# Kernel optimization log

Measured on AMD Instinct MI355X. Metric: run time of the kernel, lower is better.

The kernel has to match this reference:

```python
import jax, jax.numpy as jnp
import numpy as np

KERNEL_NUM = 21
SIGMA = 0.1
EXACT_SIGMA = 0.001

def _kernel_params():
    mus, sigmas = [], []
    for i in range(KERNEL_NUM):
        mu = 1.0 / (KERNEL_NUM - 1) + 2.0 * i / (KERNEL_NUM - 1) - 1.0
        sigma = SIGMA
        if mu > 1.0:
            sigma = EXACT_SIGMA
            mu = 1.0
        mus.append(mu)
        sigmas.append(sigma)
    return np.asarray(mus, np.float32), np.asarray(sigmas, np.float32)

MU, SIG = _kernel_params()  # [K], [K]

def setup_inputs() -> dict:
    key = jax.random.key(0)
    k = jax.random.split(key, 8)
    V, D, B, L, R = 50000, 128, 512, 30, 200
    emb = jax.random.normal(k[0], (V, D), dtype=jnp.float32)
    W = jax.random.normal(k[1], (1, KERNEL_NUM), dtype=jnp.float32) * 0.1
    b = jax.random.normal(k[2], (1,), dtype=jnp.float32) * 0.1
    query1 = jax.random.randint(k[3], (B, L), 0, V, dtype=jnp.int32)
    doc1 = jax.random.randint(k[4], (B, R), 0, V, dtype=jnp.int32)
    query2 = jax.random.randint(k[5], (B, L), 0, V, dtype=jnp.int32)
    doc2 = jax.random.randint(k[6], (B, R), 0, V, dtype=jnp.int32)
    return {"emb": emb, "W": W, "b": b, "query1": query1, "doc1": doc1,
            "query2": query2, "doc2": doc2}

def _l2norm(x):
    # F.normalize(p=2, dim=-1): x / max(||x||, eps)
    n = jnp.sqrt(jnp.sum(x * x, axis=-1, keepdims=True))
    return x / jnp.maximum(n, 1e-12)

def _predict(emb, W, b, q, d):
    eq = _l2norm(emb[q])              # [B,L,D]
    ed = _l2norm(emb[d])              # [B,R,D]
    M = jnp.einsum('bld,brd->blr', eq, ed)  # matching matrix [B,L,R]
    # multi-Gaussian kernel bank: [B,L,R,K]
    Kmat = jnp.exp(-0.5 * (M[..., None] - MU) ** 2 / (SIG ** 2))
    km = jnp.sum(jnp.log1p(jnp.sum(Kmat, axis=2)), axis=1)  # [B,K]
    return km @ W.T + b               # [B,1]

def reference(emb, W, b, query1, doc1, query2, doc2):
    logits1 = _predict(emb, W, b, query1, doc1)
    logits2 = _predict(emb, W, b, query2, doc2)
    return jax.nn.sigmoid(logits1 - logits2)
```

## Files before the change

kernel.cpp:

```cpp
#include <hip/hip_runtime.h>
#include <math.h>

#define V   50000
#define DIM 128
#define BB  512
#define LQ  30
#define RD  200
#define KN  21

typedef unsigned short ushort_t;
typedef __attribute__((ext_vector_type(8))) short bf16x8;
typedef __attribute__((ext_vector_type(4))) float f32x4;
typedef __attribute__((ext_vector_type(2))) float f32x2;

#if __has_builtin(__builtin_amdgcn_exp2f)
#define EXP2F(x) __builtin_amdgcn_exp2f(x)
#else
#define EXP2F(x) __expf((x) * 0.69314718f)
#endif

#define ALPHA 72.1347520f
#define E10   22026.4657948f

static __device__ __forceinline__ ushort_t f2bf(float x) {
    unsigned u = __builtin_bit_cast(unsigned, x);
    return (ushort_t)((u + 0x7FFFu + ((u >> 16) & 1u)) >> 16);
}
static __device__ __forceinline__ bf16x8 as_frag(int4 v) {
    return __builtin_bit_cast(bf16x8, v);
}

__global__ __launch_bounds__(256) void knrm_norm(const float* __restrict__ emb,
                                                 ushort_t* __restrict__ nh) {
    int row = blockIdx.x * 8 + (threadIdx.x >> 5);
    int c4  = (threadIdx.x & 31) * 4;
    const float4 v = *reinterpret_cast<const float4*>(emb + (size_t)row * DIM + c4);
    float ss = v.x * v.x + v.y * v.y + v.z * v.z + v.w * v.w;
#pragma unroll
    for (int off = 1; off < 32; off <<= 1) ss += __shfl_xor(ss, off);
    float inv = 1.0f / fmaxf(sqrtf(ss), 1e-12f);
    uint2 o;
    o.x = (unsigned)f2bf(v.x * inv) | ((unsigned)f2bf(v.y * inv) << 16);
    o.y = (unsigned)f2bf(v.z * inv) | ((unsigned)f2bf(v.w * inv) << 16);
    *reinterpret_cast<uint2*>(nh + (size_t)row * DIM + c4) = o;
}

static __device__ __forceinline__ void bank4_pk(f32x4 pv, int4 dt, int qt,
                                                f32x2* ks2, float& cnt) {
    const float mv[4] = {pv[0], pv[1], pv[2], pv[3]};
    const int   dv[4] = {dt.x, dt.y, dt.z, dt.w};
    f32x2 t[4], u[4];
#pragma unroll
    for (int i = 0; i < 4; ++i) {
        float m  = mv[i];
        float dA = m + 0.5f, dB = m - 0.5f;
        float tA = EXP2F(-ALPHA * dA * (dA + 0.9f));
        float tB = EXP2F(-ALPHA * dB * (dB + 0.9f));
        float uB = EXP2F(14.4269504f * dB);
        float uA = uB * E10;
        t[i] = f32x2{tA, tB};
        u[i] = f32x2{uA, uB};
        cnt += (dv[i] == qt) ? 1.0f : 0.0f;
    }
#pragma unroll
    for (int k = 0; k < 10; ++k) {
        ks2[k] += (t[0] + t[1]) + (t[2] + t[3]);
        t[0] *= u[0]; t[1] *= u[1]; t[2] *= u[2]; t[3] *= u[3];
    }
}

static __device__ __forceinline__ void load_frag4(const ushort_t* base, int4* f) {
    f[0] = *reinterpret_cast<const int4*>(base);
    f[1] = *reinterpret_cast<const int4*>(base + 32);
    f[2] = *reinterpret_cast<const int4*>(base + 64);
    f[3] = *reinterpret_cast<const int4*>(base + 96);
}

__global__ __launch_bounds__(256, 4) void knrm_main(
    const ushort_t* __restrict__ nh, const float* __restrict__ W,
    const int* __restrict__ q1, const int* __restrict__ d1,
    const int* __restrict__ q2, const int* __restrict__ d2,
    float* __restrict__ logits)
{
    __shared__ int sQtok[32];
    __shared__ __align__(16) int sDtok[256];
    __shared__ float kred[4][32][KN];

    const int pb = blockIdx.x;
    const int pair = pb >> 9, b = pb & 511;
    const int* qind = (pair ? q2 : q1) + b * LQ;
    const int* dind = (pair ? d2 : d1) + b * RD;

    const int tid = threadIdx.x;
    const int lane = tid & 63, w = tid >> 6;
    const int r = lane & 15, g = lane >> 4;

    if (tid < 32) sQtok[tid] = (tid < LQ) ? qind[tid] : -2;
    { int c = tid; sDtok[c] = (c < RD) ? dind[c] : -1; }

    const int qiA = qind[r];
    const int qiB = qind[(16 + r) < LQ ? (16 + r) : LQ - 1];
    int4 qa[4], qb[4];
    load_frag4(nh + (size_t)qiA * DIM + g * 8, qa);
    load_frag4(nh + (size_t)qiB * DIM + g * 8, qb);

    __syncthreads();

    const int qt0 = sQtok[r], qt1 = sQtok[16 + r];
    const int4* sDtok4 = (const int4*)sDtok;

    f32x2 ks0[10], ks1[10];
#pragma unroll
    for (int k = 0; k < 10; ++k) { ks0[k] = f32x2{0.f, 0.f}; ks1[k] = f32x2{0.f, 0.f}; }
    float cnt0 = 0.0f, cnt1 = 0.0f;

    const int ns = (w < 3) ? 4 : 1;
#pragma unroll 2
    for (int s = 0; s < ns; ++s) {
        const int sbase = w * 64 + s * 16;
        const int dcol = sbase + r;
        const int di = sDtok[dcol < RD ? dcol : RD - 1];

        int4 df[4];
        load_frag4(nh + (size_t)di * DIM + g * 8, df);

        f32x4 acc0 = {0.f, 0.f, 0.f, 0.f}, acc1 = {0.f, 0.f, 0.f, 0.f};
#pragma unroll
        for (int ks = 0; ks < 4; ++ks) {
            bf16x8 fd = as_frag(df[ks]);
            acc0 = __builtin_amdgcn_mfma_f32_16x16x32_bf16(fd, as_frag(qa[ks]), acc0, 0, 0, 0);
            acc1 = __builtin_amdgcn_mfma_f32_16x16x32_bf16(fd, as_frag(qb[ks]), acc1, 0, 0, 0);
        }

        if (sbase + g * 4 < RD) {
            const int4 dt = sDtok4[(sbase >> 2) + g];
            bank4_pk(acc0, dt, qt0, ks0, cnt0);
            bank4_pk(acc1, dt, qt1, ks1, cnt1);
        }
    }

#pragma unroll
    for (int k = 0; k < 10; ++k) {
        float a0 = ks0[k].x, b0 = ks0[k].y, a1 = ks1[k].x, b1 = ks1[k].y;
        a0 += __shfl_xor(a0, 16); a0 += __shfl_xor(a0, 32);
        b0 += __shfl_xor(b0, 16); b0 += __shfl_xor(b0, 32);
        a1 += __shfl_xor(a1, 16); a1 += __shfl_xor(a1, 32);
        b1 += __shfl_xor(b1, 16); b1 += __shfl_xor(b1, 32);
        ks0[k] = f32x2{a0, b0};
        ks1[k] = f32x2{a1, b1};
    }
    cnt0 += __shfl_xor(cnt0, 16); cnt0 += __shfl_xor(cnt0, 32);
    cnt1 += __shfl_xor(cnt1, 16); cnt1 += __shfl_xor(cnt1, 32);

    if (lane < 16) {
        float* k0 = &kred[w][r][0];
        float* k1 = &kred[w][16 + r][0];
#pragma unroll
        for (int k = 0; k < 10; ++k) {
            k0[k] = ks0[k].x;  k0[10 + k] = ks0[k].y;
            k1[k] = ks1[k].x;  k1[10 + k] = ks1[k].y;
        }
        k0[20] = cnt0;
        k1[20] = cnt1;
    }
    __syncthreads();

    if (lane < 32 && tid < 64) {  }
    if (tid < 64) {
        float part = 0.0f;
        if (tid < LQ) {
#pragma unroll
            for (int k = 0; k < KN; ++k) {
                float s = kred[0][tid][k] + kred[1][tid][k]
                        + kred[2][tid][k] + kred[3][tid][k];
                float sc = 1.0f;
                if (k < 20) {
                    float j = (float)((k < 10) ? k : k - 10) - 4.5f;
                    sc = EXP2F(-0.721347520f * j * j);
                }
                part += W[k] * log1pf(sc * s);
            }
        }
        part += __shfl_xor(part, 1);
        part += __shfl_xor(part, 2);
        part += __shfl_xor(part, 4);
        part += __shfl_xor(part, 8);
        part += __shfl_xor(part, 16);
        part += __shfl_xor(part, 32);
        if (tid == 0) logits[pair * BB + b] = part;
    }
}

__global__ void knrm_final(const float* __restrict__ logits, float* __restrict__ out) {
    int i = blockIdx.x * blockDim.x + threadIdx.x;
    if (i < BB) {
        float x = logits[i] - logits[BB + i];
        out[i] = 1.0f / (1.0f + expf(-x));
    }
}

extern "C" void kernel_launch(void* const* d_in, const int* in_sizes, int n_in,
                              void* d_out, int out_size, void* d_ws, size_t ws_size,
                              hipStream_t stream) {
    const float* emb = (const float*)d_in[0];
    const float* W   = (const float*)d_in[1];
    const int* q1    = (const int*)d_in[3];
    const int* dd1   = (const int*)d_in[4];
    const int* q2    = (const int*)d_in[5];
    const int* dd2   = (const int*)d_in[6];

    ushort_t* nh  = (ushort_t*)d_ws;
    float* logits = (float*)(nh + (size_t)V * DIM);

    knrm_norm<<<V / 8, 256, 0, stream>>>(emb, nh);
    knrm_main<<<1024, 256, 0, stream>>>(nh, W, q1, dd1, q2, dd2, logits);
    knrm_final<<<2, 256, 0, stream>>>(logits, (float*)d_out);
}
```

Measured before the change: 41.08 us.

## Fuse embedding normalization into main kernel and switch MFMA to fp16

Removes the separate pass that normalized the entire 50000-row embedding table to bf16. Only the gathered rows are now normalized, inside the matching kernel: each fp32 row is loaded, its squared norm is reduced across lanes, it is packed to fp16, and it is scaled by the reciprocal norm. The MFMA changes from bf16 to fp16. This drops a full-table read and write that covered far more rows than are used, at the cost of reading twice as many bytes per gathered row and doing extra arithmetic on repeated rows.

```diff
diff --git a/kernel.cpp b/kernel.cpp
--- a/kernel.cpp
+++ b/kernel.cpp
@@ -1,4 +1,5 @@
 #include <hip/hip_runtime.h>
+#include <hip/hip_fp16.h>
 #include <math.h>
 
 #define V   50000
@@ -8,8 +9,7 @@
 #define RD  200
 #define KN  21
 
-typedef unsigned short ushort_t;
-typedef __attribute__((ext_vector_type(8))) short bf16x8;
+typedef __attribute__((ext_vector_type(8))) _Float16 f16x8;
 typedef __attribute__((ext_vector_type(4))) float f32x4;
 typedef __attribute__((ext_vector_type(2))) float f32x2;
 
@@ -22,27 +22,41 @@
 #define ALPHA 72.1347520f
 #define E10   22026.4657948f
 
-static __device__ __forceinline__ ushort_t f2bf(float x) {
-    unsigned u = __builtin_bit_cast(unsigned, x);
-    return (ushort_t)((u + 0x7FFFu + ((u >> 16) & 1u)) >> 16);
-}
-static __device__ __forceinline__ bf16x8 as_frag(int4 v) {
-    return __builtin_bit_cast(bf16x8, v);
-}
-
-__global__ __launch_bounds__(256) void knrm_norm(const float* __restrict__ emb,
-                                                 ushort_t* __restrict__ nh) {
-    int row = blockIdx.x * 8 + (threadIdx.x >> 5);
-    int c4  = (threadIdx.x & 31) * 4;
-    const float4 v = *reinterpret_cast<const float4*>(emb + (size_t)row * DIM + c4);
-    float ss = v.x * v.x + v.y * v.y + v.z * v.z + v.w * v.w;
-#pragma unroll
-    for (int off = 1; off < 32; off <<= 1) ss += __shfl_xor(ss, off);
-    float inv = 1.0f / fmaxf(sqrtf(ss), 1e-12f);
-    uint2 o;
-    o.x = (unsigned)f2bf(v.x * inv) | ((unsigned)f2bf(v.y * inv) << 16);
-    o.y = (unsigned)f2bf(v.z * inv) | ((unsigned)f2bf(v.w * inv) << 16);
-    *reinterpret_cast<uint2*>(nh + (size_t)row * DIM + c4) = o;
+static __device__ __forceinline__ f16x8 as_hfrag(int4 v) {
+    return __builtin_bit_cast(f16x8, v);
+}
+static __device__ __forceinline__ unsigned pk2h(float a, float b) {
+    return __builtin_bit_cast(unsigned, __builtin_amdgcn_cvt_pkrtz(a, b));
+}
+static __device__ __forceinline__ unsigned hscale(unsigned u, __half2 s) {
+    return __builtin_bit_cast(unsigned, __hmul2(__builtin_bit_cast(__half2, u), s));
+}
+
+static __device__ __forceinline__ void gather_row_f16(const float* __restrict__ rowp,
+                                                      int g, int4* f) {
+    float ss = 0.0f;
+#pragma unroll
+    for (int ks = 0; ks < 4; ++ks) {
+        const float4* p = reinterpret_cast<const float4*>(rowp + ks * 32 + g * 8);
+        float4 a = p[0], b = p[1];
+        ss = fmaf(a.x, a.x, fmaf(a.y, a.y, fmaf(a.z, a.z, fmaf(a.w, a.w, ss))));
+        ss = fmaf(b.x, b.x, fmaf(b.y, b.y, fmaf(b.z, b.z, fmaf(b.w, b.w, ss))));
+        f[ks].x = (int)pk2h(a.x, a.y);
+        f[ks].y = (int)pk2h(a.z, a.w);
+        f[ks].z = (int)pk2h(b.x, b.y);
+        f[ks].w = (int)pk2h(b.z, b.w);
+    }
+    ss += __shfl_xor(ss, 16);
+    ss += __shfl_xor(ss, 32);
+    const float inv = rsqrtf(fmaxf(ss, 1e-24f));
+    const __half2 h2 = __float2half2_rn(inv);
+#pragma unroll
+    for (int ks = 0; ks < 4; ++ks) {
+        f[ks].x = (int)hscale((unsigned)f[ks].x, h2);
+        f[ks].y = (int)hscale((unsigned)f[ks].y, h2);
+        f[ks].z = (int)hscale((unsigned)f[ks].z, h2);
+        f[ks].w = (int)hscale((unsigned)f[ks].w, h2);
+    }
 }
 
 static __device__ __forceinline__ void bank4_pk(f32x4 pv, int4 dt, int qt,
@@ -69,15 +83,8 @@
     }
 }
 
-static __device__ __forceinline__ void load_frag4(const ushort_t* base, int4* f) {
-    f[0] = *reinterpret_cast<const int4*>(base);
-    f[1] = *reinterpret_cast<const int4*>(base + 32);
-    f[2] = *reinterpret_cast<const int4*>(base + 64);
-    f[3] = *reinterpret_cast<const int4*>(base + 96);
-}
-
 __global__ __launch_bounds__(256, 4) void knrm_main(
-    const ushort_t* __restrict__ nh, const float* __restrict__ W,
+    const float* __restrict__ emb, const float* __restrict__ W,
     const int* __restrict__ q1, const int* __restrict__ d1,
     const int* __restrict__ q2, const int* __restrict__ d2,
     float* __restrict__ logits)
@@ -101,8 +108,8 @@
     const int qiA = qind[r];
     const int qiB = qind[(16 + r) < LQ ? (16 + r) : LQ - 1];
     int4 qa[4], qb[4];
-    load_frag4(nh + (size_t)qiA * DIM + g * 8, qa);
-    load_frag4(nh + (size_t)qiB * DIM + g * 8, qb);
+    gather_row_f16(emb + (size_t)qiA * DIM, g, qa);
+    gather_row_f16(emb + (size_t)qiB * DIM, g, qb);
 
     __syncthreads();
 
@@ -122,14 +129,14 @@
         const int di = sDtok[dcol < RD ? dcol : RD - 1];
 
         int4 df[4];
-        load_frag4(nh + (size_t)di * DIM + g * 8, df);
+        gather_row_f16(emb + (size_t)di * DIM, g, df);
 
         f32x4 acc0 = {0.f, 0.f, 0.f, 0.f}, acc1 = {0.f, 0.f, 0.f, 0.f};
 #pragma unroll
         for (int ks = 0; ks < 4; ++ks) {
-            bf16x8 fd = as_frag(df[ks]);
-            acc0 = __builtin_amdgcn_mfma_f32_16x16x32_bf16(fd, as_frag(qa[ks]), acc0, 0, 0, 0);
-            acc1 = __builtin_amdgcn_mfma_f32_16x16x32_bf16(fd, as_frag(qb[ks]), acc1, 0, 0, 0);
+            f16x8 fd = as_hfrag(df[ks]);
+            acc0 = __builtin_amdgcn_mfma_f32_16x16x32_f16(fd, as_hfrag(qa[ks]), acc0, 0, 0, 0);
+            acc1 = __builtin_amdgcn_mfma_f32_16x16x32_f16(fd, as_hfrag(qb[ks]), acc1, 0, 0, 0);
         }
 
         if (sbase + g * 4 < RD) {
@@ -165,7 +172,6 @@
     }
     __syncthreads();
 
-    if (lane < 32 && tid < 64) {  }
     if (tid < 64) {
         float part = 0.0f;
         if (tid < LQ) {
@@ -209,10 +215,8 @@
     const int* q2    = (const int*)d_in[5];
     const int* dd2   = (const int*)d_in[6];
 
-    ushort_t* nh  = (ushort_t*)d_ws;
-    float* logits = (float*)(nh + (size_t)V * DIM);
-
-    knrm_norm<<<V / 8, 256, 0, stream>>>(emb, nh);
-    knrm_main<<<1024, 256, 0, stream>>>(nh, W, q1, dd1, q2, dd2, logits);
+    float* logits = (float*)d_ws;
+
+    knrm_main<<<1024, 256, 0, stream>>>(emb, W, q1, dd1, q2, dd2, logits);
     knrm_final<<<2, 256, 0, stream>>>(logits, (float*)d_out);
 }
```

Result: faster. 38.23 us (-6.9%).
